# Kernel optimization log

Hardware: AMD Instinct MI355X
Metric: run time of the kernel (lower is better)

The kernel has to match this reference:

```python
import jax, jax.numpy as jnp
import numpy as np
import math

B, N, D = 4, 2048, 512
H, DH = 8, 128
INNER = H * DH


def setup_inputs() -> dict:
    key = jax.random.key(0)
    k1, k2, k3, k4 = jax.random.split(key, 4)
    x = jax.random.normal(k1, (B, N, D), dtype=jnp.float32)
    Wg = jax.random.normal(k2, (D, INNER), dtype=jnp.float32) * (1.0 / math.sqrt(D))
    Wout = jax.random.normal(k3, (INNER, D), dtype=jnp.float32) * (1.0 / math.sqrt(INNER))
    sigma = jax.random.uniform(k4, (1, H, 1, 1), dtype=jnp.float32, minval=0.5, maxval=2.5)
    return {"x": x, "Wg": Wg, "Wout": Wout, "sigma": sigma}


def reference(x, Wg, Wout, sigma):
    b, n, d = x.shape
    h, dh = H, DH
    # value projection: [b,n,d] @ [d, h*dh] -> [b,h,n,dh]
    v = (x @ Wg).reshape(b, n, h, dh).transpose(0, 2, 1, 3)
    # fixed Gaussian positional mask, shared across batch: build once per head
    pos = jnp.arange(1, n + 1, dtype=jnp.float32)
    diffs = jnp.abs(pos[:, None] - pos[None, :])  # [n, n]
    sig = sigma.reshape(h, 1, 1)  # [h,1,1]
    inv_norm = 1.0 / (jnp.sqrt(2.0 * jnp.float32(math.pi)) * sig)
    gauss = inv_norm * jnp.exp(-(diffs[None] ** 2) / (2.0 * sig ** 2))  # [h,n,n]
    corr = gauss / gauss.sum(-1, keepdims=True)  # row-normalized [h,n,n]
    # attention: broadcast mask over batch
    attn = jnp.einsum('hnm,bhmd->bhnd', corr, v)
    out = attn.transpose(0, 2, 1, 3).reshape(b, n, h * dh)
    return out @ Wout  # dropout p=0.0 -> identity
```

## Files before the change

kernel.cpp:

```cpp
#include <hip/hip_runtime.h>
#include <hip/hip_bf16.h>
#include <math.h>

#define B_ 4
#define N_ 2048
#define D_ 512
#define H_ 8
#define DH_ 128
#define INNER_ 1024
#define W_ 32
#define M_ (B_ * N_)

typedef __attribute__((ext_vector_type(8))) short short8;
typedef __attribute__((ext_vector_type(4))) float floatx4;

typedef const __attribute__((address_space(1))) char* gcp;
typedef __attribute__((address_space(3))) char* lcp;

__device__ __forceinline__ unsigned f_to_bf16bits(float f) {
    union { float f; unsigned u; } c; c.f = f;
    return (c.u + 0x7fffu + ((c.u >> 16) & 1u)) >> 16;
}
__device__ __forceinline__ float bf16s_to_f(unsigned short s) {
    union { unsigned u; float f; } c; c.u = ((unsigned)s) << 16; return c.f;
}

#define VST 136

__global__ __launch_bounds__(256, 4) void g1_blur(
    const __hip_bfloat16* __restrict__ x_bf,
    const __hip_bfloat16* __restrict__ Wg_t,
    const float* __restrict__ sigma,
    __hip_bfloat16* __restrict__ attn)
{
    __shared__ char smem[35328];
    __hip_bfloat16* Asm = (__hip_bfloat16*)smem;
    __hip_bfloat16* Bsm = (__hip_bfloat16*)(smem + 16384);

    const int tid  = threadIdx.x;
    const int lane = tid & 63;
    const int w    = tid >> 6;
    const int wm   = w >> 1;
    const int wn   = w & 1;
    const int quad = lane >> 4;
    const int cl   = lane & 15;
    const int bm   = blockIdx.x;
    const int h    = blockIdx.y;
    const int n0   = bm * 64;
    const int nb0  = n0 & (N_ - 1);

    floatx4 acc[4][4];
    #pragma unroll
    for (int i = 0; i < 4; ++i)
        #pragma unroll
        for (int j = 0; j < 4; ++j) acc[i][j] = (floatx4){0.f, 0.f, 0.f, 0.f};

    const char* Ab = (const char*)x_bf;
    const char* Bb = (const char*)(Wg_t + (size_t)(h * DH_) * D_);

    for (int k0 = 0; k0 < D_; k0 += 64) {
        #pragma unroll
        for (int it = 0; it < 4; ++it) {
            int o = it * 4096 + tid * 16;
            int r = o >> 7;
            int s = (o >> 4) & 7;
            int c = s ^ (r & 7);
            int gr = n0 - W_ + r;
            gr = gr < 0 ? 0 : (gr > M_ - 1 ? M_ - 1 : gr);
            __builtin_amdgcn_global_load_lds(
                (gcp)(Ab + (size_t)gr * 1024 + k0 * 2 + c * 16), (lcp)(smem + o), 16, 0, 0);
            __builtin_amdgcn_global_load_lds(
                (gcp)(Bb + (size_t)r * 1024 + k0 * 2 + c * 16), (lcp)(smem + 16384 + o), 16, 0, 0);
        }
        __syncthreads();

        const short* As = (const short*)Asm;
        const short* Bs = (const short*)Bsm;
        #pragma unroll
        for (int kk = 0; kk < 2; ++kk) {
            short8 af[4], bf[4];
            int ch = kk * 4 + quad;
            #pragma unroll
            for (int t = 0; t < 4; ++t) {
                int ra = wm * 64 + t * 16 + cl;
                int rb = wn * 64 + t * 16 + cl;
                af[t] = *(const short8*)(As + ra * 64 + ((ch ^ (ra & 7)) * 8));
                bf[t] = *(const short8*)(Bs + rb * 64 + ((ch ^ (rb & 7)) * 8));
            }
            #pragma unroll
            for (int i = 0; i < 4; ++i)
                #pragma unroll
                for (int j = 0; j < 4; ++j)
                    acc[i][j] = __builtin_amdgcn_mfma_f32_16x16x32_bf16(
                        af[i], bf[j], acc[i][j], 0, 0, 0);
        }
        __syncthreads();
    }

    unsigned short* vsT   = (unsigned short*)smem;
    unsigned short* wtabS = (unsigned short*)(smem + 34816);
    float*          winv  = (float*)(smem + 35072);

    #pragma unroll
    for (int i = 0; i < 4; ++i) {
        #pragma unroll
        for (int j = 0; j < 4; ++j) {
            int ch   = wn * 64 + j * 16 + cl;
            int row0 = wm * 64 + i * 16 + quad * 4;
            unsigned p01 = 0u, p23 = 0u;
            #pragma unroll
            for (int rr = 0; rr < 4; ++rr) {
                int vb = nb0 - W_ + row0 + rr;
                unsigned bits = (vb >= 0 && vb < N_) ? f_to_bf16bits(acc[i][j][rr]) : 0u;
                if (rr < 2) p01 |= bits << (rr * 16);
                else        p23 |= bits << ((rr - 2) * 16);
            }
            unsigned* dst = (unsigned*)(vsT + ch * VST + row0);
            dst[0] = p01; dst[1] = p23;
        }
    }
    if (tid <= 2 * W_) {
        float sig = sigma[h];
        float d = (float)(tid - W_);
        wtabS[tid] = (unsigned short)f_to_bf16bits(__expf(-d * d / (2.0f * sig * sig)));
    }
    __syncthreads();

    if (tid < 64) {
        float ws = 0.f;
        #pragma unroll
        for (int l = 0; l <= 2 * W_; ++l) {
            int vb = nb0 + tid + l - W_;
            ws += (vb >= 0 && vb < N_) ? bf16s_to_f(wtabS[l]) : 0.f;
        }
        winv[tid] = 1.0f / ws;
    }

    short afr[2][4][8];
    #pragma unroll
    for (int mi = 0; mi < 2; ++mi) {
        int row = wm * 32 + mi * 16 + cl;
        #pragma unroll
        for (int k4 = 0; k4 < 4; ++k4) {
            int lb = k4 * 32 + quad * 8 - row;
            #pragma unroll
            for (int j = 0; j < 8; ++j) {
                int l = lb + j;
                afr[mi][k4][j] = (l >= 0 && l <= 2 * W_) ? (short)wtabS[l] : (short)0;
            }
        }
    }
    __syncthreads();

    floatx4 oacc[2][4];
    #pragma unroll
    for (int mi = 0; mi < 2; ++mi)
        #pragma unroll
        for (int ni = 0; ni < 4; ++ni) oacc[mi][ni] = (floatx4){0.f, 0.f, 0.f, 0.f};

    #pragma unroll
    for (int k4 = 0; k4 < 4; ++k4) {
        short8 bfr[4];
        #pragma unroll
        for (int ni = 0; ni < 4; ++ni) {
            int ch = wn * 64 + ni * 16 + cl;
            bfr[ni] = *(const short8*)((const short*)vsT + ch * VST + k4 * 32 + quad * 8);
        }
        #pragma unroll
        for (int mi = 0; mi < 2; ++mi)
            #pragma unroll
            for (int ni = 0; ni < 4; ++ni)
                oacc[mi][ni] = __builtin_amdgcn_mfma_f32_16x16x32_bf16(
                    *(short8*)afr[mi][k4], bfr[ni], oacc[mi][ni], 0, 0, 0);
    }

    float wv[2][4];
    #pragma unroll
    for (int mi = 0; mi < 2; ++mi)
        #pragma unroll
        for (int r = 0; r < 4; ++r)
            wv[mi][r] = winv[wm * 32 + mi * 16 + quad * 4 + r];

    #pragma unroll
    for (int mi = 0; mi < 2; ++mi) {
        #pragma unroll
        for (int ni = 0; ni < 4; ++ni) {
            int ch = wn * 64 + ni * 16 + cl;
            #pragma unroll
            for (int r = 0; r < 4; ++r) {
                int orow = wm * 32 + mi * 16 + quad * 4 + r;
                attn[(size_t)(n0 + orow) * INNER_ + h * DH_ + ch] =
                    __float2bfloat16(oacc[mi][ni][r] * wv[mi][r]);
            }
        }
    }
}

__global__ __launch_bounds__(256, 4) void gemm2_dbuf(
    const __hip_bfloat16* __restrict__ A,
    const __hip_bfloat16* __restrict__ Bt,
    float* __restrict__ C)
{
    __shared__ char smem[32768];

    const int bid  = blockIdx.x;
    const int xcd  = bid & 7;
    const int idx  = bid >> 3;
    const int bm   = xcd * 16 + (idx & 15);
    const int bn   = idx >> 4;

    const int tid  = threadIdx.x;
    const int lane = tid & 63;
    const int w    = tid >> 6;
    const int wm   = w >> 1;
    const int wn   = w & 1;
    const int kh   = lane >> 4;
    const int ml   = lane & 15;

    floatx4 acc[2][2];
    #pragma unroll
    for (int i = 0; i < 2; ++i)
        #pragma unroll
        for (int j = 0; j < 2; ++j) acc[i][j] = (floatx4){0.f, 0.f, 0.f, 0.f};

    const char* Ab = (const char*)(A + (size_t)(bm * 64) * INNER_);
    const char* Bb = (const char*)(Bt + (size_t)(bn * 64) * INNER_);

    auto issue = [&](int buf, int k0) {
        #pragma unroll
        for (int it = 0; it < 2; ++it) {
            int o = it * 4096 + tid * 16;
            int r = o >> 7;
            int s = (o >> 4) & 7;
            int c = s ^ (r & 7);
            size_t goff = (size_t)r * 2048 + (size_t)k0 * 2 + c * 16;
            __builtin_amdgcn_global_load_lds((gcp)(Ab + goff),
                (lcp)(smem + buf * 16384 + o), 16, 0, 0);
            __builtin_amdgcn_global_load_lds((gcp)(Bb + goff),
                (lcp)(smem + buf * 16384 + 8192 + o), 16, 0, 0);
        }
    };
    auto consume = [&](int buf) {
        const short* As = (const short*)(smem + buf * 16384);
        const short* Bs = (const short*)(smem + buf * 16384 + 8192);
        short8 af[2][2], bf[2][2];
        #pragma unroll
        for (int t = 0; t < 2; ++t) {
            int ra = wm * 32 + t * 16 + ml;
            int rb = wn * 32 + t * 16 + ml;
            #pragma unroll
            for (int kk = 0; kk < 2; ++kk) {
                int ch = kk * 4 + kh;
                af[t][kk] = *(const short8*)(As + ra * 64 + ((ch ^ (ra & 7)) * 8));
                bf[t][kk] = *(const short8*)(Bs + rb * 64 + ((ch ^ (rb & 7)) * 8));
            }
        }
        #pragma unroll
        for (int kk = 0; kk < 2; ++kk)
            #pragma unroll
            for (int i = 0; i < 2; ++i)
                #pragma unroll
                for (int j = 0; j < 2; ++j)
                    acc[i][j] = __builtin_amdgcn_mfma_f32_16x16x32_bf16(
                        af[i][kk], bf[j][kk], acc[i][j], 0, 0, 0);
    };

    const int nk = INNER_ >> 6;
    issue(0, 0);
    for (int kt = 0; kt < nk; kt += 2) {
        __syncthreads();
        if (kt + 1 < nk) issue(1, (kt + 1) << 6);
        consume(0);
        __syncthreads();
        if (kt + 2 < nk) issue(0, (kt + 2) << 6);
        consume(1);
    }
    __syncthreads();

    float* Cs = (float*)smem;
    const int rq = lane >> 4;
    const int cl = lane & 15;
    #pragma unroll
    for (int i = 0; i < 2; ++i)
        #pragma unroll
        for (int j = 0; j < 2; ++j)
            #pragma unroll
            for (int r = 0; r < 4; ++r)
                Cs[(wm * 32 + i * 16 + rq * 4 + r) * 64 + wn * 32 + j * 16 + cl] = acc[i][j][r];
    __syncthreads();

    #pragma unroll
    for (int p = 0; p < 4; ++p) {
        int idx2 = p * 256 + tid;
        int rr = idx2 >> 4;
        int cc = (idx2 & 15) * 4;
        float4 vv = *(const float4*)(Cs + rr * 64 + cc);
        *(float4*)(C + (size_t)(bm * 64 + rr) * D_ + bn * 64 + cc) = vv;
    }
}

__device__ __forceinline__ void transpose32(
    const float* __restrict__ src, __hip_bfloat16* __restrict__ dst,
    int R, int Cn, int rt, int ct, int tid)
{
    __shared__ float t[32][33];
    int c0 = ct * 32, r0 = rt * 32;
    int lx = tid & 31, ly = tid >> 5;
    #pragma unroll
    for (int i = 0; i < 32; i += 8)
        t[ly + i][lx] = src[(size_t)(r0 + ly + i) * Cn + c0 + lx];
    __syncthreads();
    #pragma unroll
    for (int i = 0; i < 32; i += 8)
        dst[(size_t)(c0 + ly + i) * R + r0 + lx] = __float2bfloat16(t[lx][ly + i]);
}

__global__ __launch_bounds__(256) void prep(
    const float* __restrict__ x, const float* __restrict__ Wg,
    const float* __restrict__ Wout, __hip_bfloat16* __restrict__ x_bf,
    __hip_bfloat16* __restrict__ Wg_t, __hip_bfloat16* __restrict__ Wout_t)
{
    const int bid = blockIdx.x;
    const int tid = threadIdx.x;
    if (bid < 2048) {
        int i = bid * 256 + tid;
        const float4* s = (const float4*)x + (size_t)i * 2;
        float4 a = s[0], b = s[1];
        __hip_bfloat16 o[8] = {
            __float2bfloat16(a.x), __float2bfloat16(a.y), __float2bfloat16(a.z), __float2bfloat16(a.w),
            __float2bfloat16(b.x), __float2bfloat16(b.y), __float2bfloat16(b.z), __float2bfloat16(b.w)};
        *(short8*)(x_bf + (size_t)i * 8) = *(short8*)o;
    } else if (bid < 2560) {
        int id2 = bid - 2048;
        transpose32(Wg, Wg_t, D_, INNER_, id2 >> 5, id2 & 31, tid);
    } else {
        int id2 = bid - 2560;
        transpose32(Wout, Wout_t, INNER_, D_, id2 >> 4, id2 & 15, tid);
    }
}

extern "C" void kernel_launch(void* const* d_in, const int* in_sizes, int n_in,
                              void* d_out, int out_size, void* d_ws, size_t ws_size,
                              hipStream_t stream) {
    const float* x     = (const float*)d_in[0];
    const float* Wg    = (const float*)d_in[1];
    const float* Wout  = (const float*)d_in[2];
    const float* sigma = (const float*)d_in[3];
    float* out = (float*)d_out;

    char* ws = (char*)d_ws;
    __hip_bfloat16* x_bf   = (__hip_bfloat16*)ws;
    __hip_bfloat16* Wg_t   = (__hip_bfloat16*)(ws + (((size_t)8)  << 20));
    __hip_bfloat16* Wout_t = (__hip_bfloat16*)(ws + (((size_t)9)  << 20));
    __hip_bfloat16* attn   = (__hip_bfloat16*)(ws + (((size_t)10) << 20));

    prep<<<dim3(3072), dim3(256), 0, stream>>>(x, Wg, Wout, x_bf, Wg_t, Wout_t);

    g1_blur<<<dim3(M_ / 64, H_), dim3(256), 0, stream>>>(x_bf, Wg_t, sigma, attn);

    gemm2_dbuf<<<dim3(1024), dim3(256), 0, stream>>>(attn, Wout_t, out);
}
```

Measured before the change: 114.6 us.

## Widen gemm2 tile to 64x128 and remap g1_blur blocks for XCD locality

The output GEMM now uses 64x128 tiles, with each wave computing 32x64 through 2x4 MFMA accumulators. That halves the grid to 512 blocks and improves reuse of the A tile loaded into LDS. The change raises LDS to 48KB and lowers launch bounds occupancy to 3. Separately, g1_blur remaps its block index so consecutive row blocks for the same head land on the same XCD, which is meant to improve L2 reuse of Wg.

```diff
diff --git a/kernel.cpp b/kernel.cpp
--- a/kernel.cpp
+++ b/kernel.cpp
@@ -44,8 +44,12 @@
     const int wn   = w & 1;
     const int quad = lane >> 4;
     const int cl   = lane & 15;
-    const int bm   = blockIdx.x;
-    const int h    = blockIdx.y;
+
+    const int L    = blockIdx.x + 128 * blockIdx.y;
+    const int xcd  = L & 7;
+    const int idx  = L >> 3;
+    const int bm   = xcd * 16 + (idx & 15);
+    const int h    = idx >> 4;
     const int n0   = bm * 64;
     const int nb0  = n0 & (N_ - 1);
 
@@ -196,12 +200,12 @@
     }
 }
 
-__global__ __launch_bounds__(256, 4) void gemm2_dbuf(
+__global__ __launch_bounds__(256, 3) void gemm2_dbuf(
     const __hip_bfloat16* __restrict__ A,
     const __hip_bfloat16* __restrict__ Bt,
     float* __restrict__ C)
 {
-    __shared__ char smem[32768];
+    __shared__ char smem[49152];
 
     const int bid  = blockIdx.x;
     const int xcd  = bid & 7;
@@ -217,42 +221,55 @@
     const int kh   = lane >> 4;
     const int ml   = lane & 15;
 
-    floatx4 acc[2][2];
+    floatx4 acc[2][4];
     #pragma unroll
     for (int i = 0; i < 2; ++i)
         #pragma unroll
-        for (int j = 0; j < 2; ++j) acc[i][j] = (floatx4){0.f, 0.f, 0.f, 0.f};
+        for (int j = 0; j < 4; ++j) acc[i][j] = (floatx4){0.f, 0.f, 0.f, 0.f};
 
     const char* Ab = (const char*)(A + (size_t)(bm * 64) * INNER_);
-    const char* Bb = (const char*)(Bt + (size_t)(bn * 64) * INNER_);
+    const char* Bb = (const char*)(Bt + (size_t)(bn * 128) * INNER_);
 
     auto issue = [&](int buf, int k0) {
         #pragma unroll
         for (int it = 0; it < 2; ++it) {
             int o = it * 4096 + tid * 16;
             int r = o >> 7;
-            int s = (o >> 4) & 7;
-            int c = s ^ (r & 7);
-            size_t goff = (size_t)r * 2048 + (size_t)k0 * 2 + c * 16;
-            __builtin_amdgcn_global_load_lds((gcp)(Ab + goff),
-                (lcp)(smem + buf * 16384 + o), 16, 0, 0);
-            __builtin_amdgcn_global_load_lds((gcp)(Bb + goff),
-                (lcp)(smem + buf * 16384 + 8192 + o), 16, 0, 0);
+            int c = ((o >> 4) & 7) ^ (r & 7);
+            __builtin_amdgcn_global_load_lds(
+                (gcp)(Ab + (size_t)r * 2048 + k0 * 2 + c * 16),
+                (lcp)(smem + buf * 24576 + o), 16, 0, 0);
+        }
+        #pragma unroll
+        for (int it = 0; it < 4; ++it) {
+            int o = it * 4096 + tid * 16;
+            int r = o >> 7;
+            int c = ((o >> 4) & 7) ^ (r & 7);
+            __builtin_amdgcn_global_load_lds(
+                (gcp)(Bb + (size_t)r * 2048 + k0 * 2 + c * 16),
+                (lcp)(smem + buf * 24576 + 8192 + o), 16, 0, 0);
         }
     };
     auto consume = [&](int buf) {
-        const short* As = (const short*)(smem + buf * 16384);
-        const short* Bs = (const short*)(smem + buf * 16384 + 8192);
-        short8 af[2][2], bf[2][2];
+        const short* As = (const short*)(smem + buf * 24576);
+        const short* Bs = (const short*)(smem + buf * 24576 + 8192);
+        short8 af[2][2], bf[4][2];
         #pragma unroll
         for (int t = 0; t < 2; ++t) {
             int ra = wm * 32 + t * 16 + ml;
-            int rb = wn * 32 + t * 16 + ml;
             #pragma unroll
             for (int kk = 0; kk < 2; ++kk) {
                 int ch = kk * 4 + kh;
                 af[t][kk] = *(const short8*)(As + ra * 64 + ((ch ^ (ra & 7)) * 8));
-                bf[t][kk] = *(const short8*)(Bs + rb * 64 + ((ch ^ (rb & 7)) * 8));
+            }
+        }
+        #pragma unroll
+        for (int ni = 0; ni < 4; ++ni) {
+            int rb = wn * 64 + ni * 16 + ml;
+            #pragma unroll
+            for (int kk = 0; kk < 2; ++kk) {
+                int ch = kk * 4 + kh;
+                bf[ni][kk] = *(const short8*)(Bs + rb * 64 + ((ch ^ (rb & 7)) * 8));
             }
         }
         #pragma unroll
@@ -260,7 +277,7 @@
             #pragma unroll
             for (int i = 0; i < 2; ++i)
                 #pragma unroll
-                for (int j = 0; j < 2; ++j)
+                for (int j = 0; j < 4; ++j)
                     acc[i][j] = __builtin_amdgcn_mfma_f32_16x16x32_bf16(
                         af[i][kk], bf[j][kk], acc[i][j], 0, 0, 0);
     };
@@ -283,19 +300,19 @@
     #pragma unroll
     for (int i = 0; i < 2; ++i)
         #pragma unroll
-        for (int j = 0; j < 2; ++j)
+        for (int j = 0; j < 4; ++j)
             #pragma unroll
             for (int r = 0; r < 4; ++r)
-                Cs[(wm * 32 + i * 16 + rq * 4 + r) * 64 + wn * 32 + j * 16 + cl] = acc[i][j][r];
-    __syncthreads();
-
-    #pragma unroll
-    for (int p = 0; p < 4; ++p) {
+                Cs[(wm * 32 + i * 16 + rq * 4 + r) * 128 + wn * 64 + j * 16 + cl] = acc[i][j][r];
+    __syncthreads();
+
+    #pragma unroll
+    for (int p = 0; p < 8; ++p) {
         int idx2 = p * 256 + tid;
-        int rr = idx2 >> 4;
-        int cc = (idx2 & 15) * 4;
-        float4 vv = *(const float4*)(Cs + rr * 64 + cc);
-        *(float4*)(C + (size_t)(bm * 64 + rr) * D_ + bn * 64 + cc) = vv;
+        int rr = idx2 >> 5;
+        int cc = (idx2 & 31) * 4;
+        float4 vv = *(const float4*)(Cs + rr * 128 + cc);
+        *(float4*)(C + (size_t)(bm * 64 + rr) * D_ + bn * 128 + cc) = vv;
     }
 }
 
@@ -358,5 +375,5 @@
 
     g1_blur<<<dim3(M_ / 64, H_), dim3(256), 0, stream>>>(x_bf, Wg_t, sigma, attn);
 
-    gemm2_dbuf<<<dim3(1024), dim3(256), 0, stream>>>(attn, Wout_t, out);
-}
+    gemm2_dbuf<<<dim3(512), dim3(256), 0, stream>>>(attn, Wout_t, out);
+}
```

New measurement: 113.0 us (median of 2 runs). No clear change (-1.4%).
